# Optimization experiments

Measured on AMD Instinct MI355X. Metric: run time of the kernel, lower is better.

## Reference

```python
import jax, jax.numpy as jnp
import numpy as np
from jax import lax

B, C, H, W = 8, 64, 256, 256
GROUPS, EPS = 8, 1e-5


def setup_inputs() -> dict:
    key = jax.random.key(0)
    ks = jax.random.split(key, 7)
    scale = 1.0 / np.sqrt(C)
    return {
        "x": jax.random.normal(ks[0], (B, C, H, W), dtype=jnp.float32),
        "gn_w": jnp.ones((C,), dtype=jnp.float32),
        "gn_b": jnp.zeros((C,), dtype=jnp.float32),
        "gate_w": jax.random.normal(ks[1], (C, C), dtype=jnp.float32) * scale,
        "gate_b": jnp.zeros((C,), dtype=jnp.float32),
        "upd_w": jax.random.normal(ks[2], (C, C), dtype=jnp.float32) * scale,
        "upd_b": jnp.zeros((C,), dtype=jnp.float32),
    }


def _group_norm(x, w, b):
    b_, c, h, wd = x.shape
    xg = x.reshape(b_, GROUPS, c // GROUPS, h, wd)
    mu = xg.mean(axis=(2, 3, 4), keepdims=True)
    var = xg.var(axis=(2, 3, 4), keepdims=True)
    xn = ((xg - mu) * lax.rsqrt(var + EPS)).reshape(b_, c, h, wd)
    return xn * w[None, :, None, None] + b[None, :, None, None]


def _gated_scan(gate_f, u_f):
    # gate_f, u_f: [T, ...]; s_t = g_t * s_{t-1} + (1 - g_t) * u_t, s_{-1} = 0
    def step(s, gu):
        g, u = gu
        s = g * s + (1.0 - g) * u
        return s, s
    _, ys = lax.scan(step, jnp.zeros_like(u_f[0]), (gate_f, u_f))
    return ys


def reference(x, gn_w, gn_b, gate_w, gate_b, upd_w, upd_b):
    h = _group_norm(x, gn_w, gn_b)
    # 1x1 convs as channel contractions
    gate = jax.nn.sigmoid(jnp.einsum('oc,bchw->bohw', gate_w, h) + gate_b[None, :, None, None])
    u = jnp.einsum('oc,bchw->bohw', upd_w, h) + upd_b[None, :, None, None]
    # column scan over W: carry [B, C, H]
    hw = _gated_scan(gate.transpose(3, 0, 1, 2), u.transpose(3, 0, 1, 2))  # [W,B,C,H]
    hw = hw.transpose(1, 2, 3, 0)  # [B,C,H,W]
    # row scan over H: carry [B, C, W]
    hh = _gated_scan(gate.transpose(2, 0, 1, 3), hw.transpose(2, 0, 1, 3))  # [H,B,C,W]
    hh = hh.transpose(1, 2, 0, 3)  # [B,C,H,W]
    return x + hh
```

## Files before the change

kernel.cpp:

```cpp
#include <hip/hip_runtime.h>
#include <stdint.h>

#define BB   8
#define CC   64
#define HH   256
#define WW   256
#define HWSZ (HH*WW)
#define CHW  (CC*HH*WW)
#define GROUPELEMS (8*HWSZ)
#define EPSV 1e-5f

#define WS_PART_OFF   0
#define WS_AFF_OFF    4096
#define WS_WFRAG_OFF  8192

typedef __attribute__((ext_vector_type(8))) short bf16x8;
typedef __attribute__((ext_vector_type(4))) float f32x4;
typedef __attribute__((ext_vector_type(4))) unsigned int u32x4;
union U32x4 { uint32_t u[4]; uint4 q; bf16x8 v; u32x4 nv; };

__device__ __forceinline__ uint32_t f32_to_bf16_bits(float f) {
    uint32_t u = __float_as_uint(f);
    u += 0x7fffu + ((u >> 16) & 1u);
    return u >> 16;
}

__global__ __launch_bounds__(256) void k_stats_partial(
        const float* __restrict__ x, float2* __restrict__ part,
        const float* __restrict__ gw, const float* __restrict__ uw,
        uint32_t* __restrict__ wfrag) {
    int blk = blockIdx.x;
    int t = threadIdx.x;
    if (blk < 16) {
        int idx = blk * 256 + t;
        int fi = idx >> 8, rem = idx & 255;
        int l = rem >> 2, d = rem & 3;
        int mt = fi >> 1, s = fi & 1;
        int m = 16 * mt + (l & 15);
        int k = 32 * s + 8 * (l >> 4) + 2 * d;
        const float* Wr = (m < 64) ? (gw + m * 64) : (uw + (m - 64) * 64);
        wfrag[idx] = f32_to_bf16_bits(Wr[k]) | (f32_to_bf16_bits(Wr[k + 1]) << 16);
    }
    const float4* p = (const float4*)(x + (size_t)blk * 65536);
    float s = 0.f, s2 = 0.f;
#pragma unroll 16
    for (int i = 0; i < 64; ++i) {
        float4 v = p[t + i * 256];
        s  += v.x + v.y + v.z + v.w;
        s2 += v.x * v.x + v.y * v.y + v.z * v.z + v.w * v.w;
    }
#pragma unroll
    for (int off = 32; off; off >>= 1) {
        s  += __shfl_down(s,  off, 64);
        s2 += __shfl_down(s2, off, 64);
    }
    __shared__ float2 red[4];
    int wid = t >> 6;
    if ((t & 63) == 0) red[wid] = make_float2(s, s2);
    __syncthreads();
    if (t == 0) {
        float a = 0.f, b2 = 0.f;
#pragma unroll
        for (int i = 0; i < 4; ++i) { a += red[i].x; b2 += red[i].y; }
        part[blk] = make_float2(a, b2);
    }
}

__global__ __launch_bounds__(512) void k_stats_final(
        const float2* __restrict__ part,
        const float* __restrict__ gn_w, const float* __restrict__ gn_b,
        float2* __restrict__ aff) {
    __shared__ float2 st[64];
    int t = threadIdx.x;
    if (t < 64) {
        float s = 0.f, s2 = 0.f;
#pragma unroll
        for (int i = 0; i < 8; ++i) { float2 p = part[t * 8 + i]; s += p.x; s2 += p.y; }
        float inv  = 1.0f / (float)GROUPELEMS;
        float mu   = s * inv;
        float var  = s2 * inv - mu * mu;
        st[t] = make_float2(mu, rsqrtf(var + EPSV));
    }
    __syncthreads();
    int b = t >> 6, c = t & 63, g = c >> 3;
    float2 mr = st[b * 8 + g];
    float a  = mr.y * gn_w[c];
    aff[t] = make_float2(a, gn_b[c] - mr.x * a);
}

__global__ __launch_bounds__(256, 4) void k_row(
        const float* __restrict__ x,
        const uint32_t* __restrict__ wfrag,
        const float* __restrict__ gate_b, const float* __restrict__ upd_b,
        const float2* __restrict__ aff,
        uint32_t* __restrict__ pair) {
    __shared__ uint32_t gvhn[128 * 65];
    __shared__ float2 affs[64];
    __shared__ __align__(16) float bgs[64];
    __shared__ __align__(16) float bus[64];

    const int t = threadIdx.x;
    const int w = t >> 6, l = t & 63, q = l >> 4, r16 = l & 15;
    const int row = blockIdx.x;
    const int b = row >> 8, y = row & 255;
    const size_t rowoff = (size_t)b * CHW + (size_t)y * WW;

    if (t < 64) { affs[t] = aff[b * 64 + t]; bgs[t] = gate_b[t]; bus[t] = upd_b[t]; }
    __syncthreads();

    float s_carry = 0.f;
    for (int tau = 0; tau < 2; ++tau) {
        const int x0 = tau << 7;
#pragma unroll
        for (int i = 0; i < 4; ++i) {
            int unit = i * 256 + t;
            int c2 = unit >> 5, p4 = unit & 31;
            int c = c2 << 1, px = p4 << 2;
            const float* xp = x + rowoff + (size_t)c * HWSZ + x0 + px;
            float4 v0 = *(const float4*)xp;
            float4 v1 = *(const float4*)(xp + HWSZ);
            float2 a0 = affs[c], a1 = affs[c + 1];
            uint32_t base = px * 65 + c2;
            gvhn[base]       = f32_to_bf16_bits(v0.x * a0.x + a0.y)
                             | (f32_to_bf16_bits(v1.x * a1.x + a1.y) << 16);
            gvhn[base + 65]  = f32_to_bf16_bits(v0.y * a0.x + a0.y)
                             | (f32_to_bf16_bits(v1.y * a1.x + a1.y) << 16);
            gvhn[base + 130] = f32_to_bf16_bits(v0.z * a0.x + a0.y)
                             | (f32_to_bf16_bits(v1.z * a1.x + a1.y) << 16);
            gvhn[base + 195] = f32_to_bf16_bits(v0.w * a0.x + a0.y)
                             | (f32_to_bf16_bits(v1.w * a1.x + a1.y) << 16);
        }
        __syncthreads();

#pragma unroll
        for (int nc = 0; nc < 2; ++nc) {
            int n_local = (w << 5) + (nc << 4) + r16;
            int based = n_local * 65 + 4 * q;
            U32x4 B0u, B1u;
#pragma unroll
            for (int d = 0; d < 4; ++d) B0u.u[d] = gvhn[based + d];
#pragma unroll
            for (int d = 0; d < 4; ++d) B1u.u[d] = gvhn[based + 16 + d];
            f32x4 acc[8];
#pragma unroll
            for (int mt = 0; mt < 4; ++mt) {
                acc[mt]     = *(const f32x4*)(bgs + 16 * mt + 4 * q);
                acc[mt + 4] = *(const f32x4*)(bus + 16 * mt + 4 * q);
            }
            uintptr_t wfa = (uintptr_t)wfrag;
            asm volatile("" : "+s"(wfa));
            const uint32_t* wf = (const uint32_t*)wfa;
#pragma unroll
            for (int mt = 0; mt < 8; ++mt) {
                U32x4 a0, a1;
                a0.q = *(const uint4*)(wf + (((mt << 1) | 0) * 64 + l) * 4);
                a1.q = *(const uint4*)(wf + (((mt << 1) | 1) * 64 + l) * 4);
                acc[mt] = __builtin_amdgcn_mfma_f32_16x16x32_bf16(a0.v, B0u.v, acc[mt], 0, 0, 0);
                acc[mt] = __builtin_amdgcn_mfma_f32_16x16x32_bf16(a1.v, B1u.v, acc[mt], 0, 0, 0);
            }
#pragma unroll
            for (int mt = 0; mt < 4; ++mt)
#pragma unroll
                for (int r = 0; r < 4; ++r) {
                    float ga = acc[mt][r];
                    float ua = acc[mt + 4][r];
                    float g  = 1.0f / (1.0f + __expf(-ga));
                    float vv = (1.0f - g) * ua;
                    uint32_t pk = __builtin_amdgcn_perm(__float_as_uint(vv),
                                                        __float_as_uint(g), 0x07060302u);
                    gvhn[n_local * 65 + 16 * mt + 4 * q + r] = pk;
                }
        }
        __syncthreads();

        if (t < 64) {
            float s = s_carry;
#pragma unroll 8
            for (int xi = 0; xi < 128; ++xi) {
                uint32_t pk = gvhn[xi * 65 + t];
                float g = __uint_as_float(pk << 16);
                float v = __uint_as_float(pk & 0xffff0000u);
                s = __builtin_fmaf(g, s, v);
                gvhn[xi * 65 + t] = __builtin_amdgcn_perm(__float_as_uint(s), pk, 0x07060100u);
            }
            s_carry = s;
        }
        __syncthreads();

#pragma unroll
        for (int i = 0; i < 8; ++i) {
            int unit = i * 256 + t;
            int c = unit >> 5, p4 = unit & 31;
            int px = p4 << 2;
            uint32_t bidx = px * 65 + c;
            u32x4 o;
            o.x = gvhn[bidx];
            o.y = gvhn[bidx + 65];
            o.z = gvhn[bidx + 130];
            o.w = gvhn[bidx + 195];
            *(u32x4*)(pair + rowoff + (size_t)c * HWSZ + x0 + px) = o;
        }
        __syncthreads();
    }
}

__global__ __launch_bounds__(1024) void k_hscan2(
        uint32_t* __restrict__ io, const float* __restrict__ x) {
    __shared__ float2 gvs[4][256];
    __shared__ float  sins[4][256];
    const int t = threadIdx.x;
    const int col = t & 255, seg = t >> 8;
    const size_t base = (size_t)blockIdx.x * HWSZ + (size_t)seg * 64 * WW + col;

    float G = 1.f, V = 0.f;
    for (int grp = 0; grp < 4; ++grp) {
        uint32_t pk[16];
        size_t gb = base + (size_t)grp * 16 * WW;
#pragma unroll
        for (int j = 0; j < 16; ++j) pk[j] = io[gb + (size_t)j * WW];
#pragma unroll
        for (int j = 0; j < 16; ++j) {
            float g  = __uint_as_float(pk[j] << 16);
            float hw = __uint_as_float(pk[j] & 0xffff0000u);
            V = __builtin_fmaf(g, V, (1.f - g) * hw);
            G *= g;
        }
    }
    gvs[seg][col] = make_float2(G, V);
    __syncthreads();

    if (t < 256) {
        float s = 0.f;
#pragma unroll
        for (int sg = 0; sg < 4; ++sg) {
            sins[sg][t] = s;
            float2 gv = gvs[sg][t];
            s = __builtin_fmaf(gv.x, s, gv.y);
        }
    }
    __syncthreads();

    float s = sins[seg][col];
    uint32_t pk[16]; float xv[16];
#pragma unroll
    for (int j = 0; j < 16; ++j) pk[j] = io[base + (size_t)j * WW];
#pragma unroll
    for (int j = 0; j < 16; ++j) xv[j] = __builtin_nontemporal_load(x + base + (size_t)j * WW);
    for (int grp = 0; grp < 4; ++grp) {
        uint32_t npk[16]; float nxv[16];
        if (grp < 3) {
            size_t nb = base + (size_t)(grp + 1) * 16 * WW;
#pragma unroll
            for (int j = 0; j < 16; ++j) npk[j] = io[nb + (size_t)j * WW];
#pragma unroll
            for (int j = 0; j < 16; ++j) nxv[j] = __builtin_nontemporal_load(x + nb + (size_t)j * WW);
        }
        size_t ob = base + (size_t)grp * 16 * WW;
#pragma unroll
        for (int j = 0; j < 16; ++j) {
            float g   = __uint_as_float(pk[j] << 16);
            float hwv = __uint_as_float(pk[j] & 0xffff0000u);
            s = __builtin_fmaf(g, s, (1.f - g) * hwv);
            __builtin_nontemporal_store(__float_as_uint(xv[j] + s), io + ob + (size_t)j * WW);
        }
#pragma unroll
        for (int j = 0; j < 16; ++j) { pk[j] = npk[j]; xv[j] = nxv[j]; }
    }
}

extern "C" void kernel_launch(void* const* d_in, const int* in_sizes, int n_in,
                              void* d_out, int out_size, void* d_ws, size_t ws_size,
                              hipStream_t stream) {
    const float* x      = (const float*)d_in[0];
    const float* gn_w   = (const float*)d_in[1];
    const float* gn_b   = (const float*)d_in[2];
    const float* gate_w = (const float*)d_in[3];
    const float* gate_b = (const float*)d_in[4];
    const float* upd_w  = (const float*)d_in[5];
    const float* upd_b  = (const float*)d_in[6];

    char* ws = (char*)d_ws;
    float2*   part  = (float2*)(ws + WS_PART_OFF);
    float2*   aff   = (float2*)(ws + WS_AFF_OFF);
    uint32_t* wfrag = (uint32_t*)(ws + WS_WFRAG_OFF);
    uint32_t* pair  = (uint32_t*)d_out;

    k_stats_partial<<<512, 256, 0, stream>>>(x, part, gate_w, upd_w, wfrag);
    k_stats_final<<<1, 512, 0, stream>>>(part, gn_w, gn_b, aff);
    k_row<<<BB * HH, 256, 0, stream>>>(x, wfrag, gate_b, upd_b, aff, pair);
    k_hscan2<<<BB * CC, 1024, 0, stream>>>(pair, x);
}
```

Measured before the change: 360.6 us.

## Vectorize hscan2 to four columns per thread and keep packed data in registers

```diff
diff --git a/kernel.cpp b/kernel.cpp
--- a/kernel.cpp
+++ b/kernel.cpp
@@ -206,33 +206,37 @@
 
 __global__ __launch_bounds__(1024) void k_hscan2(
         uint32_t* __restrict__ io, const float* __restrict__ x) {
-    __shared__ float2 gvs[4][256];
-    __shared__ float  sins[4][256];
+    __shared__ float2 gvs[16][256];
+    __shared__ float  sins[16][256];
     const int t = threadIdx.x;
-    const int col = t & 255, seg = t >> 8;
-    const size_t base = (size_t)blockIdx.x * HWSZ + (size_t)seg * 64 * WW + col;
-
-    float G = 1.f, V = 0.f;
-    for (int grp = 0; grp < 4; ++grp) {
-        uint32_t pk[16];
-        size_t gb = base + (size_t)grp * 16 * WW;
-#pragma unroll
-        for (int j = 0; j < 16; ++j) pk[j] = io[gb + (size_t)j * WW];
-#pragma unroll
-        for (int j = 0; j < 16; ++j) {
-            float g  = __uint_as_float(pk[j] << 16);
-            float hw = __uint_as_float(pk[j] & 0xffff0000u);
-            V = __builtin_fmaf(g, V, (1.f - g) * hw);
-            G *= g;
-        }
-    }
-    gvs[seg][col] = make_float2(G, V);
+    const int cg = t & 63, seg = t >> 6;
+    const size_t base = (size_t)blockIdx.x * HWSZ + (size_t)seg * 16 * WW + cg * 4;
+
+    u32x4 pk[16];
+#pragma unroll
+    for (int j = 0; j < 16; ++j)
+        pk[j] = __builtin_nontemporal_load((const u32x4*)(io + base + (size_t)j * WW));
+
+    float G[4] = {1.f, 1.f, 1.f, 1.f}, V[4] = {0.f, 0.f, 0.f, 0.f};
+#pragma unroll
+    for (int j = 0; j < 16; ++j) {
+#pragma unroll
+        for (int c = 0; c < 4; ++c) {
+            uint32_t p = pk[j][c];
+            float g  = __uint_as_float(p << 16);
+            float hw = __uint_as_float(p & 0xffff0000u);
+            V[c] = __builtin_fmaf(g, V[c], (1.f - g) * hw);
+            G[c] *= g;
+        }
+    }
+#pragma unroll
+    for (int c = 0; c < 4; ++c) gvs[seg][cg * 4 + c] = make_float2(G[c], V[c]);
     __syncthreads();
 
     if (t < 256) {
         float s = 0.f;
 #pragma unroll
-        for (int sg = 0; sg < 4; ++sg) {
+        for (int sg = 0; sg < 16; ++sg) {
             sins[sg][t] = s;
             float2 gv = gvs[sg][t];
             s = __builtin_fmaf(gv.x, s, gv.y);
@@ -240,31 +244,35 @@
     }
     __syncthreads();
 
-    float s = sins[seg][col];
-    uint32_t pk[16]; float xv[16];
-#pragma unroll
-    for (int j = 0; j < 16; ++j) pk[j] = io[base + (size_t)j * WW];
-#pragma unroll
-    for (int j = 0; j < 16; ++j) xv[j] = __builtin_nontemporal_load(x + base + (size_t)j * WW);
-    for (int grp = 0; grp < 4; ++grp) {
-        uint32_t npk[16]; float nxv[16];
-        if (grp < 3) {
-            size_t nb = base + (size_t)(grp + 1) * 16 * WW;
-#pragma unroll
-            for (int j = 0; j < 16; ++j) npk[j] = io[nb + (size_t)j * WW];
-#pragma unroll
-            for (int j = 0; j < 16; ++j) nxv[j] = __builtin_nontemporal_load(x + nb + (size_t)j * WW);
-        }
-        size_t ob = base + (size_t)grp * 16 * WW;
-#pragma unroll
-        for (int j = 0; j < 16; ++j) {
-            float g   = __uint_as_float(pk[j] << 16);
-            float hwv = __uint_as_float(pk[j] & 0xffff0000u);
-            s = __builtin_fmaf(g, s, (1.f - g) * hwv);
-            __builtin_nontemporal_store(__float_as_uint(xv[j] + s), io + ob + (size_t)j * WW);
-        }
-#pragma unroll
-        for (int j = 0; j < 16; ++j) { pk[j] = npk[j]; xv[j] = nxv[j]; }
+    float s0 = sins[seg][cg * 4 + 0];
+    float s1 = sins[seg][cg * 4 + 1];
+    float s2 = sins[seg][cg * 4 + 2];
+    float s3 = sins[seg][cg * 4 + 3];
+#pragma unroll
+    for (int j = 0; j < 16; ++j) {
+        f32x4 xv = __builtin_nontemporal_load((const f32x4*)(x + base + (size_t)j * WW));
+        f32x4 res;
+        {
+            uint32_t p = pk[j][0];
+            float g = __uint_as_float(p << 16), hw = __uint_as_float(p & 0xffff0000u);
+            s0 = __builtin_fmaf(g, s0, (1.f - g) * hw); res[0] = xv[0] + s0;
+        }
+        {
+            uint32_t p = pk[j][1];
+            float g = __uint_as_float(p << 16), hw = __uint_as_float(p & 0xffff0000u);
+            s1 = __builtin_fmaf(g, s1, (1.f - g) * hw); res[1] = xv[1] + s1;
+        }
+        {
+            uint32_t p = pk[j][2];
+            float g = __uint_as_float(p << 16), hw = __uint_as_float(p & 0xffff0000u);
+            s2 = __builtin_fmaf(g, s2, (1.f - g) * hw); res[2] = xv[2] + s2;
+        }
+        {
+            uint32_t p = pk[j][3];
+            float g = __uint_as_float(p << 16), hw = __uint_as_float(p & 0xffff0000u);
+            s3 = __builtin_fmaf(g, s3, (1.f - g) * hw); res[3] = xv[3] + s3;
+        }
+        __builtin_nontemporal_store(res, (f32x4*)((float*)io + base + (size_t)j * WW));
     }
 }
 
```

Result: slower. 377.2 us (+4.6%).
